# Kernel optimization log

Measured on AMD Instinct MI355X. Metric: run time of the kernel, lower is better.

Reference implementation:

```python
import jax, jax.numpy as jnp
import numpy as np
import math

N_SCALES = 8
WAVELET_LEN = 64
MIN_SCALE, MAX_SCALE = 1.0, 64.0
BATCH, SEQ, FEAT = 16, 4096, 64


def _morlet_init():
    # Faithful to _initialize_mother_wavelets
    t = np.linspace(-4.0, 4.0, WAVELET_LEN, dtype=np.float32)
    w = np.zeros((N_SCALES, WAVELET_LEN), dtype=np.float32)
    for i in range(N_SCALES):
        omega = 2.0 + i * 0.5
        sigma = 1.0 + i * 0.1
        wav = np.exp(-t ** 2 / (2 * sigma ** 2)) * np.cos(omega * t)
        w[i] = wav / np.linalg.norm(wav)
    return jnp.asarray(w)


def setup_inputs() -> dict:
    key = jax.random.key(0)
    k1, _ = jax.random.split(key)
    signal = jax.random.normal(k1, (BATCH, SEQ, FEAT), dtype=jnp.float32)
    mother_wavelets = _morlet_init()
    scale_weights = jnp.ones((N_SCALES,), dtype=jnp.float32)
    return {"signal": signal, "mother_wavelets": mother_wavelets, "scale_weights": scale_weights}


def _scales():
    return np.logspace(math.log10(MIN_SCALE), math.log10(MAX_SCALE), N_SCALES)


def _dilate(wavelet, scale):
    # F.interpolate(mode='linear', align_corners=True) to length int(WAVELET_LEN*scale)
    L_out = int(WAVELET_LEN * scale)
    if L_out > 1:
        pos = jnp.arange(L_out, dtype=jnp.float32) * ((WAVELET_LEN - 1) / (L_out - 1))
    else:
        pos = jnp.zeros((1,), dtype=jnp.float32)
    grid = jnp.arange(WAVELET_LEN, dtype=jnp.float32)
    return jnp.interp(pos, grid, wavelet) / math.sqrt(scale)


def reference(signal, mother_wavelets, scale_weights):
    # signal: (B, S, F) -> coefficients: (B, n_scales, S, F)
    B, S, F = signal.shape
    sig = jnp.swapaxes(signal, 1, 2)  # (B, F, S): batch all FFTs over b,f per scale
    scales = _scales()
    coeffs = []
    for i in range(N_SCALES):
        s = float(scales[i])
        w = _dilate(mother_wavelets[i], s)  # (L_dil,)
        n = S + w.shape[0] - 1
        n_fft = 2 ** int(math.ceil(math.log2(n)))
        Sf = jnp.fft.rfft(sig, n=n_fft, axis=-1)
        Wf = jnp.fft.rfft(w, n=n_fft)
        conv = jnp.fft.irfft(Sf * Wf, n=n_fft, axis=-1)[..., :S]  # (B, F, S)
        coeffs.append(conv)
    C = jnp.stack(coeffs, axis=1)            # (B, n_scales, F, S)
    C = jnp.swapaxes(C, 2, 3)                # (B, n_scales, S, F)
    return C * scale_weights[None, :, None, None]
```

## Files before the change

### kernel.cpp

```cpp
#include <hip/hip_runtime.h>
#include <hip/hip_bf16.h>
#include <math.h>

typedef __attribute__((ext_vector_type(8))) short bf16x8;
typedef __attribute__((ext_vector_type(4))) float f32x4;
typedef __attribute__((ext_vector_type(4))) unsigned int u32x4;

#define NSC    8
#define SLEN   4096
#define FEAT   64
#define W_TOT  10368
#define W_TOT2 22528
#define SROW   64
#define CHUNK_B 8192

struct WavP  { int off[NSC]; int L[NSC]; float step[NSC]; float isq[NSC]; };
struct MainP { int cact[NSC]; int baseS[NSC]; };

__global__ void k_build_wav(const float* __restrict__ mw, const float* __restrict__ sw,
                            __hip_bfloat16* __restrict__ wg, WavP wp)
{
  for (int e = blockIdx.x * 256 + threadIdx.x; e < W_TOT2; e += gridDim.x * 256) {
    float val = 0.f;
    int p = 0, e2 = e;
    if (e2 >= W_TOT) { p = 1; e2 -= W_TOT; }
    if (e2 < W_TOT) {
      int s = 0;
      #pragma unroll
      for (int i = 1; i < NSC; ++i) if (e2 >= wp.off[i]) s = i;
      int x = e2 - wp.off[s] + p;
      int L = wp.L[s];
      if (x >= 97 && x <= L + 96) {
        int k = L + 96 - x;
        float pos = (float)k * wp.step[s];
        int ii = (int)pos;
        float r;
        if (ii >= 63) r = mw[s * 64 + 63];
        else {
          float a = mw[s * 64 + ii];
          r = fmaf(pos - (float)ii, mw[s * 64 + ii + 1] - a, a);
        }
        val = r * wp.isq[s] * sw[s];
      }
    }
    wg[e] = __float2bfloat16(val);
  }
}

__global__ __launch_bounds__(256) void k_transpose(const float* __restrict__ sig,
                                                   __hip_bfloat16* __restrict__ sigT2)
{
  __shared__ float t[64][65];
  const int tid = threadIdx.x;
  const float* sp = sig + (size_t)blockIdx.x * 4096;
  for (int idx = tid; idx < 4096; idx += 256)
    t[idx & 63][idx >> 6] = sp[idx];
  __syncthreads();
  __hip_bfloat16* op = sigT2 + (size_t)blockIdx.x * 4096;
  for (int idx = tid; idx < 4096; idx += 256) {
    int f = idx >> 6, rr = idx & 63;
    int dst = (f << 6) + ((((rr >> 3) ^ (f & 7)) << 3) | (rr & 7));
    op[dst] = __float2bfloat16(t[f][rr]);
  }
}

__global__ __launch_bounds__(256, 2) void k_wavelet_mfma(
    const __hip_bfloat16* __restrict__ sigT2,
    const __hip_bfloat16* __restrict__ wavg,
    float* __restrict__ out, MainP P)
{
  __shared__ __align__(16) short ldsW[W_TOT2];
  __shared__ __align__(16) short sbuf[2][64][SROW];

  const int tid = threadIdx.x;
  const int bid = blockIdx.x;
  const int tt  = 63 - (bid >> 4);
  const int b   = bid & 15;
  const int t0  = tt * 64;
  const int tw  = tid >> 6;
  const int fl  = tid & 15;
  const int g   = (tid >> 4) & 3;
  const int lanepart = 8 * g - fl;
  const int fswz = fl & 7;

  {
    const char* gp = (const char*)wavg;
    char* lp = (char*)ldsW;
    #pragma unroll
    for (int it = 0; it < 11; ++it)
      __builtin_amdgcn_global_load_lds(
        (const __attribute__((address_space(1))) void*)(gp + it * 4096 + tid * 16),
        (__attribute__((address_space(3))) void*)(lp + it * 4096 + (tid >> 6) * 1024),
        16, 0, 0);
  }

  const int C = t0 / 64 + 1;
  const char* sgbase = (const char*)(sigT2 + (size_t)(b * 64) * 4096);

  auto stage = [&](int c) {
    const char* gp = sgbase + (size_t)(t0 / 64 - c) * CHUNK_B;
    char* lp = (char*)&sbuf[c & 1][0][0];
    #pragma unroll
    for (int it = 0; it < 2; ++it)
      __builtin_amdgcn_global_load_lds(
        (const __attribute__((address_space(1))) void*)(gp + it * 4096 + tid * 16),
        (__attribute__((address_space(3))) void*)(lp + it * 4096 + (tid >> 6) * 1024),
        16, 0, 0);
  };

  f32x4 acc[NSC][4];
  const f32x4 z = {0.f, 0.f, 0.f, 0.f};
  #pragma unroll
  for (int s = 0; s < NSC; ++s)
    #pragma unroll
    for (int n = 0; n < 4; ++n) acc[s][n] = z;

  stage(0);

  for (int c = 0; c < C; ++c) {
    __syncthreads();
    if (c + 1 < C) stage(c + 1);
    const short* sb = &sbuf[c & 1][0][0];
    #pragma unroll
    for (int h = 1; h >= 0; --h) {
      const int c_old = 2 * c + 1 - h;
      const int coff = (((h << 2) + g) ^ fswz) << 3;
      bf16x8 Bf[4];
      #pragma unroll
      for (int n = 0; n < 4; ++n)
        Bf[n] = *(const bf16x8*)(sb + ((n * 16 + fl) << 6) + coff);
      const int wk = 32 - 16 * tw - 32 * c_old + lanepart;
      __builtin_amdgcn_s_setprio(1);
      #pragma unroll
      for (int s = NSC - 1; s >= 0; --s) {
        if (c_old <= P.cact[s]) {
          int yb  = P.baseS[s] + wk;
          int pr  = yb & 1;
          int idx = yb - pr + pr * W_TOT;
          const unsigned int* ap = (const unsigned int*)(ldsW + idx);
          u32x4 au;
          au.x = ap[0]; au.y = ap[1]; au.z = ap[2]; au.w = ap[3];
          bf16x8 Af = __builtin_bit_cast(bf16x8, au);
          acc[s][0] = __builtin_amdgcn_mfma_f32_16x16x32_bf16(Af, Bf[0], acc[s][0], 0, 0, 0);
          acc[s][1] = __builtin_amdgcn_mfma_f32_16x16x32_bf16(Af, Bf[1], acc[s][1], 0, 0, 0);
          acc[s][2] = __builtin_amdgcn_mfma_f32_16x16x32_bf16(Af, Bf[2], acc[s][2], 0, 0, 0);
          acc[s][3] = __builtin_amdgcn_mfma_f32_16x16x32_bf16(Af, Bf[3], acc[s][3], 0, 0, 0);
        }
      }
      __builtin_amdgcn_s_setprio(0);
    }
  }

  const int trow = t0 + tw * 16 + g * 4;
  float* ob = out + (size_t)b * NSC * SLEN * FEAT;
  #pragma unroll
  for (int s = 0; s < NSC; ++s) {
    float* os = ob + (size_t)s * SLEN * FEAT;
    #pragma unroll
    for (int n = 0; n < 4; ++n)
      #pragma unroll
      for (int r = 0; r < 4; ++r)
        os[(size_t)(trow + r) * FEAT + n * 16 + fl] = acc[s][n][r];
  }
}

extern "C" void kernel_launch(void* const* d_in, const int* in_sizes, int n_in,
                              void* d_out, int out_size, void* d_ws, size_t ws_size,
                              hipStream_t stream) {
  const float* sig = (const float*)d_in[0];
  const float* mw  = (const float*)d_in[1];
  const float* sw  = (const float*)d_in[2];
  float*       out = (float*)d_out;

  __hip_bfloat16* wavg  = (__hip_bfloat16*)d_ws;
  __hip_bfloat16* sigT2 = (__hip_bfloat16*)((char*)d_ws + 65536);

  WavP wp; MainP mp;
  const double lg = log10(64.0), st = lg / 7.0;
  int off = 0;
  for (int i = 0; i < NSC; ++i) {
    double y = (i == 7) ? lg : (double)i * st;
    double s = pow(10.0, y);
    int L = (int)(64.0 * s);
    wp.L[i]    = L;
    wp.step[i] = (float)(63.0 / (double)(L - 1));
    wp.isq[i]  = (float)(1.0 / sqrt(s));
    wp.off[i]  = off;
    mp.cact[i]  = (L + 62) >> 5;
    mp.baseS[i] = off + L + 96;
    off += ((L + 160 + 7) / 8) * 8;
  }

  k_build_wav<<<64, 256, 0, stream>>>(mw, sw, wavg, wp);
  k_transpose<<<1024, 256, 0, stream>>>(sig, sigT2);
  k_wavelet_mfma<<<1024, 256, 0, stream>>>(sigT2, wavg, out, mp);
}
```

Measured before the change: 90.95 us.

## Load signal B-fragments directly from global into registers, drop LDS staging

Removes the double-buffered LDS staging of signal chunks and the per-chunk __syncthreads, replacing them with direct global loads of bf16x8 fragments into registers, software-pipelined one half-chunk ahead. The transpose kernel no longer XOR-swizzles its output since LDS bank conflicts no longer apply. The intent is to cut barrier and LDS traffic in the main loop, at the cost of more global/L2 load latency exposed per MFMA group and higher register pressure. On the last iteration the prefetch reads one chunk before the batch's data, which stays inside the buffer for later batches but may read before the buffer's start for batch 0.

```diff
diff --git a/kernel.cpp b/kernel.cpp
--- a/kernel.cpp
+++ b/kernel.cpp
@@ -11,8 +11,6 @@
 #define FEAT   64
 #define W_TOT  10368
 #define W_TOT2 22528
-#define SROW   64
-#define CHUNK_B 8192
 
 struct WavP  { int off[NSC]; int L[NSC]; float step[NSC]; float isq[NSC]; };
 struct MainP { int cact[NSC]; int baseS[NSC]; };
@@ -57,11 +55,8 @@
     t[idx & 63][idx >> 6] = sp[idx];
   __syncthreads();
   __hip_bfloat16* op = sigT2 + (size_t)blockIdx.x * 4096;
-  for (int idx = tid; idx < 4096; idx += 256) {
-    int f = idx >> 6, rr = idx & 63;
-    int dst = (f << 6) + ((((rr >> 3) ^ (f & 7)) << 3) | (rr & 7));
-    op[dst] = __float2bfloat16(t[f][rr]);
-  }
+  for (int idx = tid; idx < 4096; idx += 256)
+    op[idx] = __float2bfloat16(t[idx >> 6][idx & 63]);
 }
 
 __global__ __launch_bounds__(256, 2) void k_wavelet_mfma(
@@ -70,7 +65,6 @@
     float* __restrict__ out, MainP P)
 {
   __shared__ __align__(16) short ldsW[W_TOT2];
-  __shared__ __align__(16) short sbuf[2][64][SROW];
 
   const int tid = threadIdx.x;
   const int bid = blockIdx.x;
@@ -81,7 +75,6 @@
   const int fl  = tid & 15;
   const int g   = (tid >> 4) & 3;
   const int lanepart = 8 * g - fl;
-  const int fswz = fl & 7;
 
   {
     const char* gp = (const char*)wavg;
@@ -93,20 +86,10 @@
         (__attribute__((address_space(3))) void*)(lp + it * 4096 + (tid >> 6) * 1024),
         16, 0, 0);
   }
+  __syncthreads();
 
-  const int C = t0 / 64 + 1;
-  const char* sgbase = (const char*)(sigT2 + (size_t)(b * 64) * 4096);
-
-  auto stage = [&](int c) {
-    const char* gp = sgbase + (size_t)(t0 / 64 - c) * CHUNK_B;
-    char* lp = (char*)&sbuf[c & 1][0][0];
-    #pragma unroll
-    for (int it = 0; it < 2; ++it)
-      __builtin_amdgcn_global_load_lds(
-        (const __attribute__((address_space(1))) void*)(gp + it * 4096 + tid * 16),
-        (__attribute__((address_space(3))) void*)(lp + it * 4096 + (tid >> 6) * 1024),
-        16, 0, 0);
-  };
+  const int C = tt + 1;
+  const __hip_bfloat16* sgb = sigT2 + ((size_t)(b * 64 + tt) << 12) + (fl << 6) + (g << 3);
 
   f32x4 acc[NSC][4];
   const f32x4 z = {0.f, 0.f, 0.f, 0.f};
@@ -115,40 +98,42 @@
     #pragma unroll
     for (int n = 0; n < 4; ++n) acc[s][n] = z;
 
-  stage(0);
+  auto compute = [&](int c_old, const bf16x8* Bf) {
+    const int wk = 32 - 16 * tw - 32 * c_old + lanepart;
+    __builtin_amdgcn_s_setprio(1);
+    #pragma unroll
+    for (int s = NSC - 1; s >= 0; --s) {
+      if (c_old <= P.cact[s]) {
+        int yb  = P.baseS[s] + wk;
+        int pr  = yb & 1;
+        int idx = yb - pr + pr * W_TOT;
+        const unsigned int* ap = (const unsigned int*)(ldsW + idx);
+        u32x4 au;
+        au.x = ap[0]; au.y = ap[1]; au.z = ap[2]; au.w = ap[3];
+        bf16x8 Af = __builtin_bit_cast(bf16x8, au);
+        acc[s][0] = __builtin_amdgcn_mfma_f32_16x16x32_bf16(Af, Bf[0], acc[s][0], 0, 0, 0);
+        acc[s][1] = __builtin_amdgcn_mfma_f32_16x16x32_bf16(Af, Bf[1], acc[s][1], 0, 0, 0);
+        acc[s][2] = __builtin_amdgcn_mfma_f32_16x16x32_bf16(Af, Bf[2], acc[s][2], 0, 0, 0);
+        acc[s][3] = __builtin_amdgcn_mfma_f32_16x16x32_bf16(Af, Bf[3], acc[s][3], 0, 0, 0);
+      }
+    }
+    __builtin_amdgcn_s_setprio(0);
+  };
+
+  bf16x8 B0[4], B1[4];
+  #pragma unroll
+  for (int n = 0; n < 4; ++n)
+    B0[n] = *(const bf16x8*)(sgb + n * 1024 + 32);
 
   for (int c = 0; c < C; ++c) {
-    __syncthreads();
-    if (c + 1 < C) stage(c + 1);
-    const short* sb = &sbuf[c & 1][0][0];
     #pragma unroll
-    for (int h = 1; h >= 0; --h) {
-      const int c_old = 2 * c + 1 - h;
-      const int coff = (((h << 2) + g) ^ fswz) << 3;
-      bf16x8 Bf[4];
-      #pragma unroll
-      for (int n = 0; n < 4; ++n)
-        Bf[n] = *(const bf16x8*)(sb + ((n * 16 + fl) << 6) + coff);
-      const int wk = 32 - 16 * tw - 32 * c_old + lanepart;
-      __builtin_amdgcn_s_setprio(1);
-      #pragma unroll
-      for (int s = NSC - 1; s >= 0; --s) {
-        if (c_old <= P.cact[s]) {
-          int yb  = P.baseS[s] + wk;
-          int pr  = yb & 1;
-          int idx = yb - pr + pr * W_TOT;
-          const unsigned int* ap = (const unsigned int*)(ldsW + idx);
-          u32x4 au;
-          au.x = ap[0]; au.y = ap[1]; au.z = ap[2]; au.w = ap[3];
-          bf16x8 Af = __builtin_bit_cast(bf16x8, au);
-          acc[s][0] = __builtin_amdgcn_mfma_f32_16x16x32_bf16(Af, Bf[0], acc[s][0], 0, 0, 0);
-          acc[s][1] = __builtin_amdgcn_mfma_f32_16x16x32_bf16(Af, Bf[1], acc[s][1], 0, 0, 0);
-          acc[s][2] = __builtin_amdgcn_mfma_f32_16x16x32_bf16(Af, Bf[2], acc[s][2], 0, 0, 0);
-          acc[s][3] = __builtin_amdgcn_mfma_f32_16x16x32_bf16(Af, Bf[3], acc[s][3], 0, 0, 0);
-        }
-      }
-      __builtin_amdgcn_s_setprio(0);
-    }
+    for (int n = 0; n < 4; ++n)
+      B1[n] = *(const bf16x8*)(sgb - c * 4096 + n * 1024);
+    compute(2 * c, B0);
+    #pragma unroll
+    for (int n = 0; n < 4; ++n)
+      B0[n] = *(const bf16x8*)(sgb - (c + 1) * 4096 + n * 1024 + 32);
+    compute(2 * c + 1, B1);
   }
 
   const int trow = t0 + tw * 16 + g * 4;
```

Measured after the change: 149.8 us. +64.7%, slower.
